# Kernel optimization log

Measured on AMD Instinct MI355X. Metric: run time of the kernel, lower is better.

Reference implementation:

```python
import jax, jax.numpy as jnp
import numpy as np

H = 128  # hidden size
I = 5    # input size


def setup_inputs() -> dict:
    key = jax.random.key(0)
    ks = jax.random.split(key, 8)
    B, T = 2048, 512
    s_ih = 1.0 / np.sqrt(H)
    x = jax.random.normal(ks[0], (B, T, I), dtype=jnp.float32)
    # PyTorch LSTM params, gate order (i, f, g, o)
    W_ih = jax.random.uniform(ks[1], (4 * H, I), jnp.float32, -s_ih, s_ih)
    W_hh = jax.random.uniform(ks[2], (4 * H, H), jnp.float32, -s_ih, s_ih)
    b_ih = jax.random.uniform(ks[3], (4 * H,), jnp.float32, -s_ih, s_ih)
    b_hh = jax.random.uniform(ks[4], (4 * H,), jnp.float32, -s_ih, s_ih)
    W_lin = jax.random.uniform(ks[5], (1, H), jnp.float32, -s_ih, s_ih)
    b_lin = jax.random.uniform(ks[6], (1,), jnp.float32, -s_ih, s_ih)
    return {"x": x, "W_ih": W_ih, "W_hh": W_hh, "b_ih": b_ih,
            "b_hh": b_hh, "W_lin": W_lin, "b_lin": b_lin}


def _lstm_final_h(x, W_ih, W_hh, b_ih, b_hh):
    B = x.shape[0]
    # Precompute input projection for all timesteps: [B, T, 4H]
    x_proj = jnp.einsum('bti,gi->btg', x, W_ih) + b_ih + b_hh

    def step(carry, xt):
        h, c = carry
        gates = xt + h @ W_hh.T  # [B, 4H]
        i, f, g, o = jnp.split(gates, 4, axis=-1)
        i = jax.nn.sigmoid(i)
        f = jax.nn.sigmoid(f)
        g = jnp.tanh(g)
        o = jax.nn.sigmoid(o)
        c = f * c + i * g
        h = o * jnp.tanh(c)
        return (h, c), None

    h0 = jnp.zeros((B, H), dtype=x.dtype)
    c0 = jnp.zeros((B, H), dtype=x.dtype)
    (h_n, _), _ = jax.lax.scan(step, (h0, c0), jnp.swapaxes(x_proj, 0, 1))
    return h_n  # [B, H]


def reference(x, W_ih, W_hh, b_ih, b_hh, W_lin, b_lin):
    h_n = _lstm_final_h(x, W_ih, W_hh, b_ih, b_hh)
    # h_n.reshape(num_layers*B, H) @ linear -> [B, 1]
    return h_n @ W_lin.T + b_lin
```

## Files before the change

### kernel.cpp

```cpp
#include <hip/hip_runtime.h>


#define HH 128
#define II 5
#define TT 512
#define BT 8
#define NT 512
#define K8S 144
#define HB8 (16 * K8S)
#define KS 136
#define XT (TT * 8 + 8)

typedef __attribute__((ext_vector_type(4))) _Float16 half4;
typedef __attribute__((ext_vector_type(4))) float f32x4;
typedef __attribute__((ext_vector_type(4))) int int4v;

#define SIG(u) __builtin_amdgcn_rcpf(1.0f + __builtin_amdgcn_exp2f(u))
#define MF16(A, B, C) __builtin_amdgcn_mfma_f32_16x16x16f16((A), (B), (C), 0, 0, 0)
#define MI8(A, B, C)  __builtin_amdgcn_mfma_i32_16x16x64_i8((A), (B), (C), 0, 0, 0)

#define INV_IFO (-1.44269504f / 130048.0f)
#define INV_G   ( 2.88539008f / 130048.0f)

#define STEP(PB, LAST) {                                                        \
    const unsigned char* hp = hrd8 + (PB) * HB8;                                \
    int4v alo = *reinterpret_cast<const int4v*>(hp);                            \
    int4v ahi = *reinterpret_cast<const int4v*>(hp + 64);                       \
           \
    f32x4 xp0 = MF16(ax4, wfx[0], zero4);                                       \
    f32x4 xp1 = MF16(ax4, wfx[1], zero4);                                       \
    f32x4 xp2 = MF16(ax4, wfx[2], zero4);                                       \
    f32x4 xp3 = MF16(ax4, wfx[3], zero4);                                       \
                                        \
    int4v s0 = MI8(alo, wq[0][0], zeroi); int4v s1 = MI8(alo, wq[1][0], zeroi); \
    s0 = MI8(ahi, wq[0][1], s0);          s1 = MI8(ahi, wq[1][1], s1);          \
          \
    float iv0 = SIG(fmaf((float)s0[0], INV_IFO, xp0[0]));                       \
    float iv1 = SIG(fmaf((float)s0[1], INV_IFO, xp0[1]));                       \
    float fv0 = SIG(fmaf((float)s1[0], INV_IFO, xp1[0]));                       \
    float fv1 = SIG(fmaf((float)s1[1], INV_IFO, xp1[1]));                       \
                                                             \
    int4v s2 = MI8(alo, wq[2][0], zeroi); int4v s3 = MI8(alo, wq[3][0], zeroi); \
    s2 = MI8(ahi, wq[2][1], s2);          s3 = MI8(ahi, wq[3][1], s3);          \
    if (!(LAST)) {                             \
        xcur += xinc;                                                           \
        ax4 = *reinterpret_cast<const half4*>(xcur);                            \
    }                                                                           \
    float gv0 = 1.0f - 2.0f * SIG(fmaf((float)s2[0], INV_G, xp2[0]));           \
    float ov0 = SIG(fmaf((float)s3[0], INV_IFO, xp3[0]));                       \
    cc0 = fv0 * cc0 + iv0 * gv0;                                                \
    float hv0 = ov0 * (1.0f - 2.0f * SIG(2.88539008f * cc0));                   \
    float gv1 = 1.0f - 2.0f * SIG(fmaf((float)s2[1], INV_G, xp2[1]));           \
    float ov1 = SIG(fmaf((float)s3[1], INV_IFO, xp3[1]));                       \
    cc1 = fv1 * cc1 + iv1 * gv1;                                                \
    float hv1 = ov1 * (1.0f - 2.0f * SIG(2.88539008f * cc1));                   \
    if (LAST) {                                                                 \
        hsc[bcell][hcol] = hv0; hsc[bcell + 1][hcol] = hv1;                     \
    } else {                                                                    \
        unsigned char* wp = hwr8 + ((PB) ^ 1) * HB8;                            \
        wp[0]    = (unsigned char)(signed char)(int)rintf(hv0 * 127.0f);        \
        wp[K8S]  = (unsigned char)(signed char)(int)rintf(hv1 * 127.0f);        \
    }                                                                           \
    __syncthreads();                                                            \
}

__global__ __launch_bounds__(NT)
__attribute__((amdgpu_waves_per_eu(2, 2)))
void lstm_r17(const float* __restrict__ x,
              const float* __restrict__ W_ih,
              const float* __restrict__ W_hh,
              const float* __restrict__ b_ih,
              const float* __restrict__ b_hh,
              const float* __restrict__ W_lin,
              const float* __restrict__ b_lin,
              float* __restrict__ out,
              int B)
{
    __shared__ __align__(16) unsigned char hb8[2][16][K8S];
    __shared__ __align__(16) _Float16 zrow[KS];
    __shared__ __align__(16) _Float16 xs[BT * XT];
    __shared__ float hsc[BT][HH + 4];

    const int tid  = threadIdx.x;
    const int b0   = blockIdx.x * BT;
    const int lane = tid & 63;
    const int w    = tid >> 6;
    const int n    = lane & 15;
    const int q    = lane >> 4;
    const int hcol = w * 16 + n;

    int4v wq[4][2];
    half4 wfx[4];
    #pragma unroll
    for (int g = 0; g < 4; ++g) {
        const float sc = (g == 2) ? 2.88539008f : -1.44269504f;
        const int j = g * HH + hcol;
        #pragma unroll
        for (int half = 0; half < 2; ++half) {
            const float* p = W_hh + (size_t)j * HH + half * 64 + q * 16;
            #pragma unroll
            for (int r = 0; r < 4; ++r) {
                int wd = 0;
                #pragma unroll
                for (int u = 0; u < 4; ++u) {
                    int b = (int)rintf(p[r * 4 + u] * 1024.0f);
                    wd |= (b & 0xff) << (8 * u);
                }
                wq[g][half][r] = wd;
            }
        }
        #pragma unroll
        for (int e = 0; e < 4; ++e) {
            const int k = q * 4 + e;
            float v = 0.0f;
            if (k < II)       v = W_ih[j * II + k];
            else if (k == II) v = b_ih[j] + b_hh[j];
            wfx[g][e] = (_Float16)(v * sc);
        }
    }

    for (int idx = tid; idx < 2 * 16 * K8S; idx += NT)
        (&hb8[0][0][0])[idx] = 0;
    if (tid < KS) zrow[tid] = (_Float16)0.0f;
    for (int idx = tid; idx < BT * XT; idx += NT)
        xs[idx] = (_Float16)0.0f;
    __syncthreads();

    {
        const int lb = tid & 63, bb = tid >> 6;
        if (b0 + bb < B) {
            const float* xb = x + (size_t)(b0 + bb) * TT * II;
            for (int e = lb * 4; e < TT * II; e += 256) {
                float4 v = *reinterpret_cast<const float4*>(xb + e);
                float vv[4] = {v.x, v.y, v.z, v.w};
                #pragma unroll
                for (int u = 0; u < 4; ++u) {
                    const int ee = e + u;
                    xs[bb * XT + (ee / 5) * 8 + (ee % 5)] = (_Float16)vv[u];
                }
            }
        }
        for (int s = tid; s < BT * TT; s += NT)
            xs[(s >> 9) * XT + (s & 511) * 8 + 5] = (_Float16)1.0f;
    }
    __syncthreads();

    const int bcell = 2 * q;
    float cc0 = 0.f, cc1 = 0.f;
    const f32x4 zero4 = {0.f, 0.f, 0.f, 0.f};
    const int4v zeroi = {0, 0, 0, 0};
    const bool xreal = ((n & 2) == 0);
    const int  bofn  = (n >> 2) * 2 + (n & 1);
    const unsigned char* hrd8 = &hb8[0][n][0] + q * 16;
    unsigned char*       hwr8 = &hb8[0][q * 4][0] + hcol;
    const _Float16* xcur = xreal ? (&xs[bofn * XT] + q * 4) : (&zrow[0] + q * 4);
    const int       xinc = xreal ? 8 : 0;

    half4 ax4 = *reinterpret_cast<const half4*>(xcur);

    #pragma unroll 1
    for (int k = 0; k < (TT - 2) / 2; ++k) {
        STEP(0, false);
        STEP(1, false);
    }
    STEP(0, false);
    STEP(1, true);

    float p = hsc[w][lane] * W_lin[lane] + hsc[w][lane + 64] * W_lin[lane + 64];
    #pragma unroll
    for (int off = 32; off > 0; off >>= 1) p += __shfl_down(p, off, 64);
    if (lane == 0 && (b0 + w) < B) out[b0 + w] = p + b_lin[0];
}

extern "C" void kernel_launch(void* const* d_in, const int* in_sizes, int n_in,
                              void* d_out, int out_size, void* d_ws, size_t ws_size,
                              hipStream_t stream) {
    const float* x     = (const float*)d_in[0];
    const float* W_ih  = (const float*)d_in[1];
    const float* W_hh  = (const float*)d_in[2];
    const float* b_ih  = (const float*)d_in[3];
    const float* b_hh  = (const float*)d_in[4];
    const float* W_lin = (const float*)d_in[5];
    const float* b_lin = (const float*)d_in[6];
    float* out = (float*)d_out;

    const int B = in_sizes[0] / (TT * II);
    const int grid = (B + BT - 1) / BT;
    lstm_r17<<<grid, NT, 0, stream>>>(x, W_ih, W_hh, b_ih, b_hh,
                                      W_lin, b_lin, out, B);
}
```

Before: 325.7 us.

## Halve batch tile to 4 and give each wave 32 hidden columns

Shrinks the per-block batch tile from 8 to 4 sequences and the block to 256 threads, doubling the grid. Each wave now owns 32 hidden columns, issuing twice as many MFMAs per step, and exchanges half-wave gate results with lane shuffles so each lane still updates two cells. The aim is to use MFMA rows that were wasted on padded batch slots and to raise the number of independent blocks in flight. In exchange, per-thread register use for weights doubles and cross-lane shuffles are added to every recurrent step.

```diff
diff --git a/kernel.cpp b/kernel.cpp
--- a/kernel.cpp
+++ b/kernel.cpp
@@ -4,8 +4,8 @@
 #define HH 128
 #define II 5
 #define TT 512
-#define BT 8
-#define NT 512
+#define BT 4
+#define NT 256
 #define K8S 144
 #define HB8 (16 * K8S)
 #define KS 136
@@ -27,35 +27,67 @@
     int4v alo = *reinterpret_cast<const int4v*>(hp);                            \
     int4v ahi = *reinterpret_cast<const int4v*>(hp + 64);                       \
            \
-    f32x4 xp0 = MF16(ax4, wfx[0], zero4);                                       \
-    f32x4 xp1 = MF16(ax4, wfx[1], zero4);                                       \
-    f32x4 xp2 = MF16(ax4, wfx[2], zero4);                                       \
-    f32x4 xp3 = MF16(ax4, wfx[3], zero4);                                       \
-                                        \
-    int4v s0 = MI8(alo, wq[0][0], zeroi); int4v s1 = MI8(alo, wq[1][0], zeroi); \
-    s0 = MI8(ahi, wq[0][1], s0);          s1 = MI8(ahi, wq[1][1], s1);          \
-          \
-    float iv0 = SIG(fmaf((float)s0[0], INV_IFO, xp0[0]));                       \
-    float iv1 = SIG(fmaf((float)s0[1], INV_IFO, xp0[1]));                       \
-    float fv0 = SIG(fmaf((float)s1[0], INV_IFO, xp1[0]));                       \
-    float fv1 = SIG(fmaf((float)s1[1], INV_IFO, xp1[1]));                       \
-                                                             \
-    int4v s2 = MI8(alo, wq[2][0], zeroi); int4v s3 = MI8(alo, wq[3][0], zeroi); \
-    s2 = MI8(ahi, wq[2][1], s2);          s3 = MI8(ahi, wq[3][1], s3);          \
+    f32x4 xp00 = MF16(ax4, wfx[0][0], zero4);                                   \
+    f32x4 xp01 = MF16(ax4, wfx[0][1], zero4);                                   \
+    f32x4 xp02 = MF16(ax4, wfx[0][2], zero4);                                   \
+    f32x4 xp03 = MF16(ax4, wfx[0][3], zero4);                                   \
+    f32x4 xp10 = MF16(ax4, wfx[1][0], zero4);                                   \
+    f32x4 xp11 = MF16(ax4, wfx[1][1], zero4);                                   \
+    f32x4 xp12 = MF16(ax4, wfx[1][2], zero4);                                   \
+    f32x4 xp13 = MF16(ax4, wfx[1][3], zero4);                                   \
     if (!(LAST)) {                             \
         xcur += xinc;                                                           \
         ax4 = *reinterpret_cast<const half4*>(xcur);                            \
     }                                                                           \
-    float gv0 = 1.0f - 2.0f * SIG(fmaf((float)s2[0], INV_G, xp2[0]));           \
-    float ov0 = SIG(fmaf((float)s3[0], INV_IFO, xp3[0]));                       \
+                          \
+    int4v s00 = MI8(alo, wq[0][0][0], zeroi);                                   \
+    int4v s01 = MI8(alo, wq[0][1][0], zeroi);                                   \
+    int4v s10 = MI8(alo, wq[1][0][0], zeroi);                                   \
+    int4v s11 = MI8(alo, wq[1][1][0], zeroi);                                   \
+    s00 = MI8(ahi, wq[0][0][1], s00);                                           \
+    s01 = MI8(ahi, wq[0][1][1], s01);                                           \
+    s10 = MI8(ahi, wq[1][0][1], s10);                                           \
+    s11 = MI8(ahi, wq[1][1][1], s11);                                           \
+                    \
+    float ai0 = fmaf((float)s00[0], INV_IFO, xp00[0]);                          \
+    float ai1 = fmaf((float)s00[1], INV_IFO, xp00[1]);                          \
+    float af0 = fmaf((float)s01[0], INV_IFO, xp01[0]);                          \
+    float af1 = fmaf((float)s01[1], INV_IFO, xp01[1]);                          \
+    float bi0 = __shfl_xor(fmaf((float)s10[0], INV_IFO, xp10[0]), 32, 64);      \
+    float bi1 = __shfl_xor(fmaf((float)s10[1], INV_IFO, xp10[1]), 32, 64);      \
+    float bf0 = __shfl_xor(fmaf((float)s11[0], INV_IFO, xp11[0]), 32, 64);      \
+    float bf1 = __shfl_xor(fmaf((float)s11[1], INV_IFO, xp11[1]), 32, 64);      \
+    float iv0 = SIG(hi ? bi0 : ai0);                                            \
+    float iv1 = SIG(hi ? bi1 : ai1);                                            \
+    float fv0 = SIG(hi ? bf0 : af0);                                            \
+    float fv1 = SIG(hi ? bf1 : af1);                                            \
+                                               \
+    int4v s02 = MI8(alo, wq[0][2][0], zeroi);                                   \
+    int4v s03 = MI8(alo, wq[0][3][0], zeroi);                                   \
+    int4v s12 = MI8(alo, wq[1][2][0], zeroi);                                   \
+    int4v s13 = MI8(alo, wq[1][3][0], zeroi);                                   \
+    s02 = MI8(ahi, wq[0][2][1], s02);                                           \
+    s03 = MI8(ahi, wq[0][3][1], s03);                                           \
+    s12 = MI8(ahi, wq[1][2][1], s12);                                           \
+    s13 = MI8(ahi, wq[1][3][1], s13);                                           \
+    float ag0 = fmaf((float)s02[0], INV_G,   xp02[0]);                          \
+    float ag1 = fmaf((float)s02[1], INV_G,   xp02[1]);                          \
+    float ao0 = fmaf((float)s03[0], INV_IFO, xp03[0]);                          \
+    float ao1 = fmaf((float)s03[1], INV_IFO, xp03[1]);                          \
+    float bg0 = __shfl_xor(fmaf((float)s12[0], INV_G,   xp12[0]), 32, 64);      \
+    float bg1 = __shfl_xor(fmaf((float)s12[1], INV_G,   xp12[1]), 32, 64);      \
+    float bo0 = __shfl_xor(fmaf((float)s13[0], INV_IFO, xp13[0]), 32, 64);      \
+    float bo1 = __shfl_xor(fmaf((float)s13[1], INV_IFO, xp13[1]), 32, 64);      \
+    float gv0 = 1.0f - 2.0f * SIG(hi ? bg0 : ag0);                              \
+    float ov0 = SIG(hi ? bo0 : ao0);                                            \
     cc0 = fv0 * cc0 + iv0 * gv0;                                                \
     float hv0 = ov0 * (1.0f - 2.0f * SIG(2.88539008f * cc0));                   \
-    float gv1 = 1.0f - 2.0f * SIG(fmaf((float)s2[1], INV_G, xp2[1]));           \
-    float ov1 = SIG(fmaf((float)s3[1], INV_IFO, xp3[1]));                       \
+    float gv1 = 1.0f - 2.0f * SIG(hi ? bg1 : ag1);                              \
+    float ov1 = SIG(hi ? bo1 : ao1);                                            \
     cc1 = fv1 * cc1 + iv1 * gv1;                                                \
     float hv1 = ov1 * (1.0f - 2.0f * SIG(2.88539008f * cc1));                   \
     if (LAST) {                                                                 \
-        hsc[bcell][hcol] = hv0; hsc[bcell + 1][hcol] = hv1;                     \
+        hsc[bcell][mycol] = hv0; hsc[bcell + 1][mycol] = hv1;                   \
     } else {                                                                    \
         unsigned char* wp = hwr8 + ((PB) ^ 1) * HB8;                            \
         wp[0]    = (unsigned char)(signed char)(int)rintf(hv0 * 127.0f);        \
@@ -66,7 +98,7 @@
 
 __global__ __launch_bounds__(NT)
 __attribute__((amdgpu_waves_per_eu(2, 2)))
-void lstm_r17(const float* __restrict__ x,
+void lstm_r19(const float* __restrict__ x,
               const float* __restrict__ W_ih,
               const float* __restrict__ W_hh,
               const float* __restrict__ b_ih,
@@ -87,41 +119,46 @@
     const int w    = tid >> 6;
     const int n    = lane & 15;
     const int q    = lane >> 4;
-    const int hcol = w * 16 + n;
-
-    int4v wq[4][2];
-    half4 wfx[4];
+    const bool hi  = (q >= 2);
+    const int qr   = q & 1;
+    const int mycol = w * 32 + (hi ? 16 : 0) + n;
+
+    int4v wq[2][4][2];
+    half4 wfx[2][4];
     #pragma unroll
-    for (int g = 0; g < 4; ++g) {
-        const float sc = (g == 2) ? 2.88539008f : -1.44269504f;
-        const int j = g * HH + hcol;
+    for (int c = 0; c < 2; ++c) {
         #pragma unroll
-        for (int half = 0; half < 2; ++half) {
-            const float* p = W_hh + (size_t)j * HH + half * 64 + q * 16;
+        for (int g = 0; g < 4; ++g) {
+            const float sc = (g == 2) ? 2.88539008f : -1.44269504f;
+            const int j = g * HH + w * 32 + c * 16 + n;
             #pragma unroll
-            for (int r = 0; r < 4; ++r) {
-                int wd = 0;
+            for (int hf = 0; hf < 2; ++hf) {
+                const float* p = W_hh + (size_t)j * HH + hf * 64 + q * 16;
                 #pragma unroll
-                for (int u = 0; u < 4; ++u) {
-                    int b = (int)rintf(p[r * 4 + u] * 1024.0f);
-                    wd |= (b & 0xff) << (8 * u);
+                for (int r = 0; r < 4; ++r) {
+                    int wd = 0;
+                    #pragma unroll
+                    for (int u = 0; u < 4; ++u) {
+                        int bq = (int)rintf(p[r * 4 + u] * 1024.0f);
+                        wd |= (bq & 0xff) << (8 * u);
+                    }
+                    wq[c][g][hf][r] = wd;
                 }
-                wq[g][half][r] = wd;
+            }
+            #pragma unroll
+            for (int e = 0; e < 4; ++e) {
+                const int k = q * 4 + e;
+                float v = 0.0f;
+                if (k < II)       v = W_ih[j * II + k];
+                else if (k == II) v = b_ih[j] + b_hh[j];
+                wfx[c][g][e] = (_Float16)(v * sc);
             }
         }
-        #pragma unroll
-        for (int e = 0; e < 4; ++e) {
-            const int k = q * 4 + e;
-            float v = 0.0f;
-            if (k < II)       v = W_ih[j * II + k];
-            else if (k == II) v = b_ih[j] + b_hh[j];
-            wfx[g][e] = (_Float16)(v * sc);
-        }
     }
 
     for (int idx = tid; idx < 2 * 16 * K8S; idx += NT)
         (&hb8[0][0][0])[idx] = 0;
-    if (tid < KS) zrow[tid] = (_Float16)0.0f;
+    for (int idx = tid; idx < KS; idx += NT) zrow[idx] = (_Float16)0.0f;
     for (int idx = tid; idx < BT * XT; idx += NT)
         xs[idx] = (_Float16)0.0f;
     __syncthreads();
@@ -145,14 +182,14 @@
     }
     __syncthreads();
 
-    const int bcell = 2 * q;
+    const int bcell = 2 * qr;
     float cc0 = 0.f, cc1 = 0.f;
     const f32x4 zero4 = {0.f, 0.f, 0.f, 0.f};
     const int4v zeroi = {0, 0, 0, 0};
-    const bool xreal = ((n & 2) == 0);
+    const bool xreal = ((n & 2) == 0) && (n < 8);
     const int  bofn  = (n >> 2) * 2 + (n & 1);
     const unsigned char* hrd8 = &hb8[0][n][0] + q * 16;
-    unsigned char*       hwr8 = &hb8[0][q * 4][0] + hcol;
+    unsigned char*       hwr8 = &hb8[0][qr * 4][0] + mycol;
     const _Float16* xcur = xreal ? (&xs[bofn * XT] + q * 4) : (&zrow[0] + q * 4);
     const int       xinc = xreal ? 8 : 0;
 
@@ -186,6 +223,6 @@
 
     const int B = in_sizes[0] / (TT * II);
     const int grid = (B + BT - 1) / BT;
-    lstm_r17<<<grid, NT, 0, stream>>>(x, W_ih, W_hh, b_ih, b_hh,
+    lstm_r19<<<grid, NT, 0, stream>>>(x, W_ih, W_hh, b_ih, b_hh,
                                       W_lin, b_lin, out, B);
 }
```

New measurement: 487.8 us. 1.5x slower.
